# Performance work log

Measured on AMD Instinct MI355X. Metric: run time of the kernel, lower is better.

## Reference

```python
import jax, jax.numpy as jnp
import numpy as np
import math

# ---- hyperparameters taken verbatim from the source losses ----
NSAMPLE_REP = 20      # ballquery nsample in get_repulsion_loss
RADIUS_REP = 0.07     # ballquery radius in get_repulsion_loss
H_REP = 0.03          # kernel bandwidth h
PERCENTAGES = (0.004, 0.008, 0.01, 0.012, 0.016)
UNI_RADIUS = 1.0


def _gather(p, idx):
    # p: [B, N, 3], idx: [B, ...] int -> [B, ..., 3]  (pointops.grouping/gathering)
    return jax.vmap(lambda pts, i: pts[i])(p, idx)


def _ballquery(radius, nsample, q, p):
    # pointops.ballquery: for each query, first `nsample` point indices within
    # radius, padded with the first found index. q:[B,M,3], p:[B,N,3] -> [B,M,nsample]
    d = jnp.sum((q[:, :, None, :] - p[:, None, :, :]) ** 2, -1)  # [B,M,N]
    N = p.shape[1]
    keys = jnp.where(d <= radius * radius,
                     jnp.arange(N, dtype=jnp.int32)[None, None, :], N)
    idx = jnp.sort(keys, axis=-1)[..., :nsample]
    return jnp.where(idx >= N, idx[..., :1], idx)  # pad misses with first hit


def _fps(pcd, npoint):
    # pointops.furthestsampling on [B,N,3] -> [B,npoint] int32
    B, N, _ = pcd.shape
    bidx = jnp.arange(B)

    def step(carry, _):
        dist, far = carry                         # [B,N], [B]
        pt = pcd[bidx, far]                       # [B,3]
        d = jnp.sum((pcd - pt[:, None, :]) ** 2, -1)
        dist = jnp.minimum(dist, d)
        nxt = jnp.argmax(dist, -1).astype(jnp.int32)
        return (dist, nxt), far

    init = (jnp.full((B, N), 1e10, pcd.dtype), jnp.zeros((B,), jnp.int32))
    _, idxs = jax.lax.scan(step, init, None, length=npoint)
    return idxs.T  # [B, npoint]


def _repulsion_loss(pred):
    # pred: [B, N, 3]
    idx = _ballquery(RADIUS_REP, NSAMPLE_REP, pred, pred)   # [B,N,20], detached ints
    g = _gather(pred, idx) - pred[:, :, None, :]            # [B,N,20,3]
    dists = jnp.sum(g * g, -1)                              # [B,N,20]
    vals, _ = jax.lax.top_k(-dists, 5)                      # 5 smallest sq-dists
    d5 = jnp.maximum(-vals[:, :, 1:], 0.0)                  # drop self, ReLU
    ds = jnp.sqrt(d5)
    w = jnp.exp(-d5 / (H_REP * H_REP))
    return jnp.mean(RADIUS_REP - ds * w)


def _uniform_loss(pcd):
    # pcd: [B, N, 3]
    N = pcd.shape[1]
    npoint = int(N * 0.05)
    # FPS is called with identical args for every percentage -> compute once.
    fps_idx = _fps(jax.lax.stop_gradient(pcd), npoint)
    new_xyz = _gather(pcd, fps_idx)                          # [B,npoint,3]
    loss = jnp.zeros((), pcd.dtype)
    for p in PERCENTAGES:
        nsample = int(N * p)
        r = math.sqrt(p * UNI_RADIUS)
        disk_area = math.pi * UNI_RADIUS ** 2 * p / nsample
        expect_len = math.sqrt(2 * disk_area / 1.732)
        idx = _ballquery(r, nsample, new_xyz, pcd)           # [B,npoint,nsample]
        grouped = _gather(pcd, idx).reshape(-1, nsample, 3)  # [B*npoint,nsample,3]
        # knn_point(2, grouped, grouped): pairwise sq-dists inside each disk
        d = jnp.sum((grouped[:, :, None, :] - grouped[:, None, :, :]) ** 2, -1)
        vals, _ = jax.lax.top_k(-d, 2)
        ud = -vals[:, :, 1:]                                  # nearest non-self sqdist
        ud = jnp.sqrt(jnp.abs(ud + 1e-8))
        ud = jnp.mean(ud, -1)
        ud = (ud - expect_len) ** 2 / (expect_len + 1e-8)
        loss = loss + jnp.mean(ud) * (p * 100.0) ** 2
    return loss / len(PERCENTAGES)


def setup_inputs() -> dict:
    key = jax.random.key(0)
    # refined upsampled cloud: B=4, r*N = 4*2048 = 8192 points in [-1,1]^3
    pcd = jax.random.uniform(key, (4, 8192, 3), jnp.float32) * 2.0 - 1.0
    return {"pcd": pcd}


def reference(pcd):
    return jnp.stack([_uniform_loss(pcd), _repulsion_loss(pcd)])
```

## Files before the change

### kernel.cpp

```cpp
#include <hip/hip_runtime.h>
#include <hip/hip_bf16.h>
#include <cmath>
#include <cfloat>

#define BATCH 4
#define NPTS 8192
#define NPOINT 409
#define NBALLS (BATCH * NPOINT)
#define REP_NS 20
#define REP_SEG 8
#define SEG_LEN (NPTS / REP_SEG)
#define REP_TASKS 512
#define NTASKS (REP_TASKS + NBALLS)
#define NWORKERS 252

#define UW 96
#define UH (8 * UW)

#define WS_FPS_OFF 0
#define WS_REP_OFF 8192
#define WS_UNI_OFF 12288
#define WS_CNT_OFF 25600

typedef float v2f __attribute__((ext_vector_type(2)));

struct UniParams {
  float  thr[5];
  float  e[5];
  float  eden[5];
  int    ns[5];
};

template <int CTRL>
__device__ __forceinline__ unsigned long long dpp_max_u64(unsigned long long key) {
  const int lo = __builtin_amdgcn_update_dpp(
      0, (int)(unsigned)(key & 0xFFFFFFFFull), CTRL, 0xf, 0xf, true);
  const int hi = __builtin_amdgcn_update_dpp(
      0, (int)(unsigned)(key >> 32), CTRL, 0xf, 0xf, true);
  const unsigned long long ok =
      ((unsigned long long)(unsigned)hi << 32) | (unsigned)lo;
  return ok > key ? ok : key;
}

__device__ __forceinline__ void ins5(float v, float& t0, float& t1, float& t2,
                                     float& t3, float& t4) {
  if (v < t4) {
    t4 = v;
    if (t4 < t3) { float tmp = t3; t3 = t4; t4 = tmp; }
    if (t3 < t2) { float tmp = t2; t2 = t3; t3 = tmp; }
    if (t2 < t1) { float tmp = t1; t1 = t2; t2 = tmp; }
    if (t1 < t0) { float tmp = t0; t0 = t1; t1 = tmp; }
  }
}

__device__ __forceinline__ float rep_term(float d) {
  d = fmaxf(d, 0.0f);
  return 0.07f - sqrtf(d) * expf(-(d / 0.0009f));
}

__global__ __launch_bounds__(512, 2) void fused_kernel(const float* __restrict__ pcd,
                                                       int* __restrict__ fps_idx,
                                                       double* __restrict__ rep_part,
                                                       double* __restrict__ uni_part,
                                                       int* __restrict__ counter,
                                                       UniParams up, float rep_thr) {
  const int tid = threadIdx.x;
  const int lane = tid & 63;
  const int w = tid >> 6;
  extern __shared__ float smem[];

  __shared__ unsigned long long s_key[2][8];
  __shared__ float s_t5[REP_SEG][64][5];
  __shared__ float s_d0[REP_SEG][64];
  __shared__ int   s_cnt[REP_SEG][64];
  __shared__ float wx[8][UW], wy[8][UW], wz[8][UW], wd[8][UW];
  __shared__ int   s_wcnt[8];
  __shared__ float FX[UH], FY[UH], FZ[UH], FD[UH];
  __shared__ float CX[5][131], CY[5][131], CZ[5][131];
  __shared__ double dpart[8];
  __shared__ int s_task, s_qidx;

  if (blockIdx.x < BATCH) {
    const int b = blockIdx.x;
    const float* P = pcd + b * NPTS * 3;
    float* X = smem;
    float* Y = smem + NPTS;
    float* Z = smem + 2 * NPTS;

    for (int i = tid; i < NPTS; i += 512) {
      X[i] = P[i * 3 + 0];
      Y[i] = P[i * 3 + 1];
      Z[i] = P[i * 3 + 2];
    }

    v2f px[8], py[8], pz[8], dist[8];
    const int base = tid * 16;
#pragma unroll
    for (int k = 0; k < 8; k++) {
      const int i0 = (base + 2 * k) * 3;
      const int i1 = (base + 2 * k + 1) * 3;
      px[k] = (v2f){P[i0 + 0], P[i1 + 0]};
      py[k] = (v2f){P[i0 + 1], P[i1 + 1]};
      pz[k] = (v2f){P[i0 + 2], P[i1 + 2]};
      dist[k] = (v2f){1e10f, 1e10f};
    }
#pragma unroll
    for (int k = 0; k < 8; k++) {
      asm volatile("" : "+v"(px[k]), "+v"(py[k]), "+v"(pz[k]));
    }

    __syncthreads();

    int far = 0;
    float fx = X[0], fy = Y[0], fz = Z[0];
    for (int s = 0; s < NPOINT; s++) {
      if (tid == 0) {
        __hip_atomic_store(&fps_idx[b * NPOINT + s], far,
                           __ATOMIC_RELAXED, __HIP_MEMORY_SCOPE_AGENT);
      }

      const v2f fxv = (v2f){fx, fx};
      const v2f fyv = (v2f){fy, fy};
      const v2f fzv = (v2f){fz, fz};
      float best = -1.0f;
      int kb = 0;
#pragma unroll
      for (int k = 0; k < 8; k++) {
#pragma clang fp contract(off)
        const v2f dx = px[k] - fxv;
        const v2f dy = py[k] - fyv;
        const v2f dz = pz[k] - fzv;
        const v2f d  = (dx * dx + dy * dy) + dz * dz;
        const float n0 = fminf(dist[k].x, d.x);
        const float n1 = fminf(dist[k].y, d.y);
        dist[k].x = n0;
        dist[k].y = n1;
        if (n0 > best) { best = n0; kb = 2 * k; }
        if (n1 > best) { best = n1; kb = 2 * k + 1; }
      }
      const int bidx = base + kb;
      unsigned long long key =
          ((unsigned long long)__float_as_uint(best) << 32) |
          (unsigned long long)(0xFFFFFFFFu - (unsigned)bidx);

      key = dpp_max_u64<0x111>(key);
      key = dpp_max_u64<0x112>(key);
      key = dpp_max_u64<0x114>(key);
      key = dpp_max_u64<0x118>(key);
      key = dpp_max_u64<0x142>(key);
      key = dpp_max_u64<0x143>(key);

      const int par = s & 1;
      if (lane == 63) s_key[par][w] = key;
      __syncthreads();
      unsigned long long kbk = s_key[par][0];
#pragma unroll
      for (int w2 = 1; w2 < 8; w2++) {
        const unsigned long long kk = s_key[par][w2];
        if (kk > kbk) kbk = kk;
      }
      far = (int)(0xFFFFFFFFu - (unsigned)(kbk & 0xFFFFFFFFull));
      fx = X[far];
      fy = Y[far];
      fz = Z[far];
    }
    return;
  }

  const double wj_tab[5] = {0.16 / (5.0 * 1636.0 * 32.0),
                            0.64 / (5.0 * 1636.0 * 65.0),
                            1.0  / (5.0 * 1636.0 * 81.0),
                            1.44 / (5.0 * 1636.0 * 98.0),
                            2.56 / (5.0 * 1636.0 * 131.0)};

  while (true) {
    __syncthreads();
    if (tid == 0) s_task = atomicAdd(counter, 1);
    __syncthreads();
    const int t = s_task;
    if (t >= NTASKS) return;

    if (t < REP_TASKS) {
      const int b = t >> 7;
      const int q = ((t & 127) << 6) + lane;
      const float* P = pcd + b * NPTS * 3;

      const float qx = P[q * 3 + 0], qy = P[q * 3 + 1], qz = P[q * 3 + 2];

      int cnt = 0;
      float d0 = 0.0f;
      float t0 = FLT_MAX, t1 = FLT_MAX, t2 = FLT_MAX, t3 = FLT_MAX, t4 = FLT_MAX;

      const int wu = __builtin_amdgcn_readfirstlane(w);
      const float* S = P + wu * SEG_LEN * 3;
#pragma unroll 4
      for (int i = 0; i < SEG_LEN; i++) {
        const float x = S[i * 3 + 0];
        const float y = S[i * 3 + 1];
        const float z = S[i * 3 + 2];
        const float dx = qx - x, dy = qy - y, dz = qz - z;
        const float d = dx * dx + dy * dy + dz * dz;
        if (d <= rep_thr && cnt < REP_NS) {
          if (cnt == 0) d0 = d;
          ins5(d, t0, t1, t2, t3, t4);
          cnt++;
        }
      }

      s_t5[w][lane][0] = t0; s_t5[w][lane][1] = t1; s_t5[w][lane][2] = t2;
      s_t5[w][lane][3] = t3; s_t5[w][lane][4] = t4;
      s_d0[w][lane] = d0;
      s_cnt[w][lane] = cnt;
      __syncthreads();

      if (w == 0) {
        int total = 0;
        float fd0 = 0.0f;
        int first_seen = 0;
        float m0 = FLT_MAX, m1 = FLT_MAX, m2 = FLT_MAX, m3 = FLT_MAX, m4 = FLT_MAX;
#pragma unroll
        for (int sg = 0; sg < REP_SEG; sg++) {
          const int c = s_cnt[sg][lane];
          if (c > 0 && !first_seen) { fd0 = s_d0[sg][lane]; first_seen = 1; }
          total += c;
#pragma unroll
          for (int j = 0; j < 5; j++) ins5(s_t5[sg][lane][j], m0, m1, m2, m3, m4);
        }

        if (total > REP_NS) {
          int c2 = 0;
          m0 = FLT_MAX; m1 = FLT_MAX; m2 = FLT_MAX; m3 = FLT_MAX; m4 = FLT_MAX;
          for (int i = 0; i < NPTS && c2 < REP_NS; i++) {
            const float dx = qx - P[i * 3 + 0];
            const float dy = qy - P[i * 3 + 1];
            const float dz = qz - P[i * 3 + 2];
            const float d = dx * dx + dy * dy + dz * dz;
            if (d <= rep_thr) { ins5(d, m0, m1, m2, m3, m4); c2++; }
          }
        } else {
          for (int c = total; c < REP_NS; c++) ins5(fd0, m0, m1, m2, m3, m4);
        }

        float sum = rep_term(m1) + rep_term(m2) + rep_term(m3) + rep_term(m4);
#pragma unroll
        for (int off = 32; off >= 1; off >>= 1) sum += __shfl_down(sum, off);
        if (lane == 0) rep_part[t] = (double)sum;
      }
    } else {
      const int ball = t - REP_TASKS;
      const int b = ball / NPOINT;
      const float* P = pcd + b * NPTS * 3;

      if (tid == 0) {
        int v = __hip_atomic_load(&fps_idx[ball], __ATOMIC_RELAXED,
                                  __HIP_MEMORY_SCOPE_AGENT);
        while (v < 0) {
          __builtin_amdgcn_s_sleep(32);
          v = __hip_atomic_load(&fps_idx[ball], __ATOMIC_RELAXED,
                                __HIP_MEMORY_SCOPE_AGENT);
        }
        s_qidx = v;
      }
      __syncthreads();
      const int qidx = s_qidx;
      const float qx = P[qidx * 3 + 0], qy = P[qidx * 3 + 1], qz = P[qidx * 3 + 2];

      int wcnt = 0;
      const float* S = P + w * 1024 * 3;
      for (int it = 0; it < 16; it++) {
        const int j = it * 64 + lane;
        const float x = S[j * 3 + 0];
        const float y = S[j * 3 + 1];
        const float z = S[j * 3 + 2];
        const float dx = qx - x, dy = qy - y, dz = qz - z;
        const float d = dx * dx + dy * dy + dz * dz;
        const bool hit = (d <= up.thr[4]);
        const unsigned long long m = __ballot(hit);
        if (hit) {
          const int pos = wcnt + __popcll(m & ((1ull << lane) - 1ull));
          if (pos < UW) {
            wx[w][pos] = x; wy[w][pos] = y; wz[w][pos] = z; wd[w][pos] = d;
          }
        }
        wcnt += __popcll(m);
      }
      if (lane == 0) s_wcnt[w] = min(wcnt, UW);
      __syncthreads();

      int off = 0;
#pragma unroll
      for (int w2 = 0; w2 < 8; w2++) {
        if (w2 == w) break;
        off += s_wcnt[w2];
      }
      for (int i = lane; i < s_wcnt[w]; i += 64) {
        FX[off + i] = wx[w][i]; FY[off + i] = wy[w][i];
        FZ[off + i] = wz[w][i]; FD[off + i] = wd[w][i];
      }
      __syncthreads();
      int c = 0;
#pragma unroll
      for (int w2 = 0; w2 < 8; w2++) c += s_wcnt[w2];

      double local = 0.0;
      if (w < 5) {
        const int jp = w;
        const float thr = up.thr[jp];
        const int nsj = up.ns[jp];

        int cnt2 = 0;
        for (int bse = 0; bse < c; bse += 64) {
          const int e = bse + lane;
          const bool pred = (e < c) && (FD[e] <= thr);
          const unsigned long long m = __ballot(pred);
          if (pred) {
            const int pos = cnt2 + __popcll(m & ((1ull << lane) - 1ull));
            if (pos < nsj) {
              CX[jp][pos] = FX[e]; CY[jp][pos] = FY[e]; CZ[jp][pos] = FZ[e];
            }
          }
          cnt2 += __popcll(m);
        }
        const int cj = min(cnt2, nsj);
        const int pads = nsj - cj;
        const int istart = (pads > 0) ? 1 : 0;

        if (pads > 0 && lane == 0) {
          const float ud = sqrtf(fabsf(1e-8f));
          const float dd = ud - up.e[jp];
          const float tt = (dd * dd) / up.eden[jp];
          local += (double)tt * wj_tab[jp] * (double)(pads + 1);
        }

        for (int r = istart + lane; r < cj; r += 64) {
          const float xi = CX[jp][r], yi = CY[jp][r], zi = CZ[jp][r];
          float m2 = FLT_MAX;
          for (int e2 = 0; e2 < cj; e2++) {
            if (e2 == r) continue;
            const float dx = xi - CX[jp][e2];
            const float dy = yi - CY[jp][e2];
            const float dz = zi - CZ[jp][e2];
            const float d = dx * dx + dy * dy + dz * dz;
            if (d < m2) m2 = d;
          }
          const float ud = sqrtf(fabsf(m2 + 1e-8f));
          const float dd = ud - up.e[jp];
          const float tt = (dd * dd) / up.eden[jp];
          local += (double)tt * wj_tab[jp];
        }
      }

#pragma unroll
      for (int o = 32; o >= 1; o >>= 1) local += __shfl_down(local, o);
      if (lane == 0) dpart[w] = local;
      __syncthreads();
      if (tid == 0) {
        double u = 0.0;
#pragma unroll
        for (int w2 = 0; w2 < 8; w2++) u += dpart[w2];
        uni_part[ball] = u;
      }
    }
  }
}

__global__ __launch_bounds__(256) void fin_kernel(const double* __restrict__ rep_part,
                                                  const double* __restrict__ uni_part,
                                                  float* __restrict__ out) {
  __shared__ double sd[256];
  const int t = threadIdx.x;
  double u = 0.0, r = 0.0;
  for (int i = t; i < NBALLS; i += 256) u += uni_part[i];
  for (int i = t; i < REP_TASKS; i += 256) r += rep_part[i];

  sd[t] = u; __syncthreads();
  for (int s = 128; s > 0; s >>= 1) { if (t < s) sd[t] += sd[t + s]; __syncthreads(); }
  const double usum = sd[0];
  __syncthreads();
  sd[t] = r; __syncthreads();
  for (int s = 128; s > 0; s >>= 1) { if (t < s) sd[t] += sd[t + s]; __syncthreads(); }

  if (t == 0) {
    out[0] = (float)usum;
    out[1] = (float)(sd[0] * (1.0 / 131072.0));
  }
}

extern "C" void kernel_launch(void* const* d_in, const int* in_sizes, int n_in,
                              void* d_out, int out_size, void* d_ws, size_t ws_size,
                              hipStream_t stream) {
  (void)in_sizes; (void)n_in; (void)out_size; (void)ws_size;
  const float* pcd = (const float*)d_in[0];
  float* out = (float*)d_out;
  int*    fps      = (int*)((char*)d_ws + WS_FPS_OFF);
  double* rep_part = (double*)((char*)d_ws + WS_REP_OFF);
  double* uni_part = (double*)((char*)d_ws + WS_UNI_OFF);
  int*    counter  = (int*)((char*)d_ws + WS_CNT_OFF);

  const float rep_thr = (float)(0.07 * 0.07);

  UniParams up;
  const double ps[5] = {0.004, 0.008, 0.01, 0.012, 0.016};
  for (int j = 0; j < 5; j++) {
    const int ns = (int)(8192.0 * ps[j]);
    const double r = sqrt(ps[j]);
    up.thr[j] = (float)(r * r);
    const double disk = M_PI * ps[j] / (double)ns;
    const double el = sqrt(2.0 * disk / 1.732);
    up.e[j] = (float)el;
    up.eden[j] = (float)(el + 1e-8);
    up.ns[j] = ns;
  }

  hipMemsetAsync(fps, 0xFF, NBALLS * sizeof(int), stream);
  hipMemsetAsync(counter, 0, sizeof(int), stream);

  static const int kDynLds = NPTS * 3 * (int)sizeof(float);
  (void)hipFuncSetAttribute((const void*)fused_kernel,
                            hipFuncAttributeMaxDynamicSharedMemorySize, kDynLds);

  fused_kernel<<<BATCH + NWORKERS, 512, kDynLds, stream>>>(pcd, fps, rep_part,
                                                           uni_part, counter,
                                                           up, rep_thr);
  fin_kernel<<<1, 256, 0, stream>>>(rep_part, uni_part, out);
}
```

Baseline: 435.9 us.

## Simplify FPS argmax reduction and fold final reduction into last block

The FPS loop now reduces only the 32-bit max distance across the wavefront with DPP, then finds the winning lane via ballot and recovers its local index with a scan. This replaces the per-element best/index tracking and the 64-bit DPP key reduction. Separately, the final-sum kernel is removed: the last block to finish, detected with an atomic counter, performs the global reduction and writes the output. This saves one kernel launch at the cost of an extra atomic and fences.

```diff
diff --git a/kernel.cpp b/kernel.cpp
--- a/kernel.cpp
+++ b/kernel.cpp
@@ -13,6 +13,7 @@
 #define REP_TASKS 512
 #define NTASKS (REP_TASKS + NBALLS)
 #define NWORKERS 252
+#define NBLOCKS (BATCH + NWORKERS)
 
 #define UW 96
 #define UH (8 * UW)
@@ -32,14 +33,10 @@
 };
 
 template <int CTRL>
-__device__ __forceinline__ unsigned long long dpp_max_u64(unsigned long long key) {
-  const int lo = __builtin_amdgcn_update_dpp(
-      0, (int)(unsigned)(key & 0xFFFFFFFFull), CTRL, 0xf, 0xf, true);
-  const int hi = __builtin_amdgcn_update_dpp(
-      0, (int)(unsigned)(key >> 32), CTRL, 0xf, 0xf, true);
-  const unsigned long long ok =
-      ((unsigned long long)(unsigned)hi << 32) | (unsigned)lo;
-  return ok > key ? ok : key;
+__device__ __forceinline__ unsigned dpp_max_u32(unsigned v) {
+  const unsigned o = (unsigned)__builtin_amdgcn_update_dpp(
+      0, (int)v, CTRL, 0xf, 0xf, true);
+  return o > v ? o : v;
 }
 
 __device__ __forceinline__ void ins5(float v, float& t0, float& t1, float& t2,
@@ -63,6 +60,7 @@
                                                        double* __restrict__ rep_part,
                                                        double* __restrict__ uni_part,
                                                        int* __restrict__ counter,
+                                                       float* __restrict__ out,
                                                        UniParams up, float rep_thr) {
   const int tid = threadIdx.x;
   const int lane = tid & 63;
@@ -77,8 +75,8 @@
   __shared__ int   s_wcnt[8];
   __shared__ float FX[UH], FY[UH], FZ[UH], FD[UH];
   __shared__ float CX[5][131], CY[5][131], CZ[5][131];
-  __shared__ double dpart[8];
-  __shared__ int s_task, s_qidx;
+  __shared__ double dpart[8], rpart[8];
+  __shared__ int s_task, s_qidx, s_last;
 
   if (blockIdx.x < BATCH) {
     const int b = blockIdx.x;
@@ -122,8 +120,6 @@
       const v2f fxv = (v2f){fx, fx};
       const v2f fyv = (v2f){fy, fy};
       const v2f fzv = (v2f){fz, fz};
-      float best = -1.0f;
-      int kb = 0;
 #pragma unroll
       for (int k = 0; k < 8; k++) {
 #pragma clang fp contract(off)
@@ -131,28 +127,46 @@
         const v2f dy = py[k] - fyv;
         const v2f dz = pz[k] - fzv;
         const v2f d  = (dx * dx + dy * dy) + dz * dz;
-        const float n0 = fminf(dist[k].x, d.x);
-        const float n1 = fminf(dist[k].y, d.y);
-        dist[k].x = n0;
-        dist[k].y = n1;
-        if (n0 > best) { best = n0; kb = 2 * k; }
-        if (n1 > best) { best = n1; kb = 2 * k + 1; }
+        dist[k].x = fminf(dist[k].x, d.x);
+        dist[k].y = fminf(dist[k].y, d.y);
       }
-      const int bidx = base + kb;
-      unsigned long long key =
-          ((unsigned long long)__float_as_uint(best) << 32) |
-          (unsigned long long)(0xFFFFFFFFu - (unsigned)bidx);
-
-      key = dpp_max_u64<0x111>(key);
-      key = dpp_max_u64<0x112>(key);
-      key = dpp_max_u64<0x114>(key);
-      key = dpp_max_u64<0x118>(key);
-      key = dpp_max_u64<0x142>(key);
-      key = dpp_max_u64<0x143>(key);
-
+
+      const float m0 = fmaxf(fmaxf(dist[0].x, dist[0].y),
+                             fmaxf(dist[1].x, dist[1].y));
+      const float m1 = fmaxf(fmaxf(dist[2].x, dist[2].y),
+                             fmaxf(dist[3].x, dist[3].y));
+      const float m2 = fmaxf(fmaxf(dist[4].x, dist[4].y),
+                             fmaxf(dist[5].x, dist[5].y));
+      const float m3 = fmaxf(fmaxf(dist[6].x, dist[6].y),
+                             fmaxf(dist[7].x, dist[7].y));
+      const float tmax = fmaxf(fmaxf(m0, m1), fmaxf(m2, m3));
+
+      const unsigned tb = __float_as_uint(tmax);
+      unsigned rb = tb;
+      rb = dpp_max_u32<0x111>(rb);
+      rb = dpp_max_u32<0x112>(rb);
+      rb = dpp_max_u32<0x114>(rb);
+      rb = dpp_max_u32<0x118>(rb);
+      rb = dpp_max_u32<0x142>(rb);
+      rb = dpp_max_u32<0x143>(rb);
+      const unsigned wb = (unsigned)__builtin_amdgcn_readlane((int)rb, 63);
+
+      const unsigned long long hit = __ballot(tb == wb);
       const int par = s & 1;
-      if (lane == 63) s_key[par][w] = key;
+      if (tb == wb && (hit & ((1ull << lane) - 1ull)) == 0ull) {
+        const float wv = __uint_as_float(wb);
+        int li = 0;
+#pragma unroll
+        for (int j = 15; j >= 0; j--) {
+          const float v = (j & 1) ? dist[j >> 1].y : dist[j >> 1].x;
+          li = (v == wv) ? j : li;
+        }
+        const unsigned bidx = (unsigned)(base + li);
+        s_key[par][w] = ((unsigned long long)wb << 32) |
+                        (unsigned long long)(0xFFFFFFFFu - bidx);
+      }
       __syncthreads();
+
       unsigned long long kbk = s_key[par][0];
 #pragma unroll
       for (int w2 = 1; w2 < 8; w2++) {
@@ -164,225 +178,231 @@
       fy = Y[far];
       fz = Z[far];
     }
-    return;
+  } else {
+    const double wj_tab[5] = {0.16 / (5.0 * 1636.0 * 32.0),
+                              0.64 / (5.0 * 1636.0 * 65.0),
+                              1.0  / (5.0 * 1636.0 * 81.0),
+                              1.44 / (5.0 * 1636.0 * 98.0),
+                              2.56 / (5.0 * 1636.0 * 131.0)};
+
+    while (true) {
+      __syncthreads();
+      if (tid == 0) s_task = atomicAdd(counter, 1);
+      __syncthreads();
+      const int t = s_task;
+      if (t >= NTASKS) break;
+
+      if (t < REP_TASKS) {
+        const int b = t >> 7;
+        const int q = ((t & 127) << 6) + lane;
+        const float* P = pcd + b * NPTS * 3;
+
+        const float qx = P[q * 3 + 0], qy = P[q * 3 + 1], qz = P[q * 3 + 2];
+
+        int cnt = 0;
+        float d0 = 0.0f;
+        float t0 = FLT_MAX, t1 = FLT_MAX, t2 = FLT_MAX, t3 = FLT_MAX, t4 = FLT_MAX;
+
+        const int wu = __builtin_amdgcn_readfirstlane(w);
+        const float* S = P + wu * SEG_LEN * 3;
+#pragma unroll 4
+        for (int i = 0; i < SEG_LEN; i++) {
+          const float x = S[i * 3 + 0];
+          const float y = S[i * 3 + 1];
+          const float z = S[i * 3 + 2];
+          const float dx = qx - x, dy = qy - y, dz = qz - z;
+          const float d = dx * dx + dy * dy + dz * dz;
+          if (d <= rep_thr && cnt < REP_NS) {
+            if (cnt == 0) d0 = d;
+            ins5(d, t0, t1, t2, t3, t4);
+            cnt++;
+          }
+        }
+
+        s_t5[w][lane][0] = t0; s_t5[w][lane][1] = t1; s_t5[w][lane][2] = t2;
+        s_t5[w][lane][3] = t3; s_t5[w][lane][4] = t4;
+        s_d0[w][lane] = d0;
+        s_cnt[w][lane] = cnt;
+        __syncthreads();
+
+        if (w == 0) {
+          int total = 0;
+          float fd0 = 0.0f;
+          int first_seen = 0;
+          float n0 = FLT_MAX, n1 = FLT_MAX, n2 = FLT_MAX, n3 = FLT_MAX, n4 = FLT_MAX;
+#pragma unroll
+          for (int sg = 0; sg < REP_SEG; sg++) {
+            const int c = s_cnt[sg][lane];
+            if (c > 0 && !first_seen) { fd0 = s_d0[sg][lane]; first_seen = 1; }
+            total += c;
+#pragma unroll
+            for (int j = 0; j < 5; j++) ins5(s_t5[sg][lane][j], n0, n1, n2, n3, n4);
+          }
+
+          if (total > REP_NS) {
+            int c2 = 0;
+            n0 = FLT_MAX; n1 = FLT_MAX; n2 = FLT_MAX; n3 = FLT_MAX; n4 = FLT_MAX;
+            for (int i = 0; i < NPTS && c2 < REP_NS; i++) {
+              const float dx = qx - P[i * 3 + 0];
+              const float dy = qy - P[i * 3 + 1];
+              const float dz = qz - P[i * 3 + 2];
+              const float d = dx * dx + dy * dy + dz * dz;
+              if (d <= rep_thr) { ins5(d, n0, n1, n2, n3, n4); c2++; }
+            }
+          } else {
+            for (int c = total; c < REP_NS; c++) ins5(fd0, n0, n1, n2, n3, n4);
+          }
+
+          float sum = rep_term(n1) + rep_term(n2) + rep_term(n3) + rep_term(n4);
+#pragma unroll
+          for (int off = 32; off >= 1; off >>= 1) sum += __shfl_down(sum, off);
+          if (lane == 0) rep_part[t] = (double)sum;
+        }
+      } else {
+        const int ball = t - REP_TASKS;
+        const int b = ball / NPOINT;
+        const float* P = pcd + b * NPTS * 3;
+
+        if (tid == 0) {
+          int v = __hip_atomic_load(&fps_idx[ball], __ATOMIC_RELAXED,
+                                    __HIP_MEMORY_SCOPE_AGENT);
+          while (v < 0) {
+            __builtin_amdgcn_s_sleep(32);
+            v = __hip_atomic_load(&fps_idx[ball], __ATOMIC_RELAXED,
+                                  __HIP_MEMORY_SCOPE_AGENT);
+          }
+          s_qidx = v;
+        }
+        __syncthreads();
+        const int qidx = s_qidx;
+        const float qx = P[qidx * 3 + 0], qy = P[qidx * 3 + 1], qz = P[qidx * 3 + 2];
+
+        int wcnt = 0;
+        const float* S = P + w * 1024 * 3;
+        for (int it = 0; it < 16; it++) {
+          const int j = it * 64 + lane;
+          const float x = S[j * 3 + 0];
+          const float y = S[j * 3 + 1];
+          const float z = S[j * 3 + 2];
+          const float dx = qx - x, dy = qy - y, dz = qz - z;
+          const float d = dx * dx + dy * dy + dz * dz;
+          const bool hitp = (d <= up.thr[4]);
+          const unsigned long long m = __ballot(hitp);
+          if (hitp) {
+            const int pos = wcnt + __popcll(m & ((1ull << lane) - 1ull));
+            if (pos < UW) {
+              wx[w][pos] = x; wy[w][pos] = y; wz[w][pos] = z; wd[w][pos] = d;
+            }
+          }
+          wcnt += __popcll(m);
+        }
+        if (lane == 0) s_wcnt[w] = min(wcnt, UW);
+        __syncthreads();
+
+        int off = 0;
+#pragma unroll
+        for (int w2 = 0; w2 < 8; w2++) {
+          if (w2 == w) break;
+          off += s_wcnt[w2];
+        }
+        for (int i = lane; i < s_wcnt[w]; i += 64) {
+          FX[off + i] = wx[w][i]; FY[off + i] = wy[w][i];
+          FZ[off + i] = wz[w][i]; FD[off + i] = wd[w][i];
+        }
+        __syncthreads();
+        int c = 0;
+#pragma unroll
+        for (int w2 = 0; w2 < 8; w2++) c += s_wcnt[w2];
+
+        double local = 0.0;
+        if (w < 5) {
+          const int jp = w;
+          const float thr = up.thr[jp];
+          const int nsj = up.ns[jp];
+
+          int cnt2 = 0;
+          for (int bse = 0; bse < c; bse += 64) {
+            const int e = bse + lane;
+            const bool pred = (e < c) && (FD[e] <= thr);
+            const unsigned long long m = __ballot(pred);
+            if (pred) {
+              const int pos = cnt2 + __popcll(m & ((1ull << lane) - 1ull));
+              if (pos < nsj) {
+                CX[jp][pos] = FX[e]; CY[jp][pos] = FY[e]; CZ[jp][pos] = FZ[e];
+              }
+            }
+            cnt2 += __popcll(m);
+          }
+          const int cj = min(cnt2, nsj);
+          const int pads = nsj - cj;
+          const int istart = (pads > 0) ? 1 : 0;
+
+          if (pads > 0 && lane == 0) {
+            const float ud = sqrtf(fabsf(1e-8f));
+            const float dd = ud - up.e[jp];
+            const float tt = (dd * dd) / up.eden[jp];
+            local += (double)tt * wj_tab[jp] * (double)(pads + 1);
+          }
+
+          for (int r = istart + lane; r < cj; r += 64) {
+            const float xi = CX[jp][r], yi = CY[jp][r], zi = CZ[jp][r];
+            float mm = FLT_MAX;
+            for (int e2 = 0; e2 < cj; e2++) {
+              if (e2 == r) continue;
+              const float dx = xi - CX[jp][e2];
+              const float dy = yi - CY[jp][e2];
+              const float dz = zi - CZ[jp][e2];
+              const float d = dx * dx + dy * dy + dz * dz;
+              if (d < mm) mm = d;
+            }
+            const float ud = sqrtf(fabsf(mm + 1e-8f));
+            const float dd = ud - up.e[jp];
+            const float tt = (dd * dd) / up.eden[jp];
+            local += (double)tt * wj_tab[jp];
+          }
+        }
+
+#pragma unroll
+        for (int o = 32; o >= 1; o >>= 1) local += __shfl_down(local, o);
+        if (lane == 0) dpart[w] = local;
+        __syncthreads();
+        if (tid == 0) {
+          double u = 0.0;
+#pragma unroll
+          for (int w2 = 0; w2 < 8; w2++) u += dpart[w2];
+          uni_part[ball] = u;
+        }
+      }
+    }
   }
 
-  const double wj_tab[5] = {0.16 / (5.0 * 1636.0 * 32.0),
-                            0.64 / (5.0 * 1636.0 * 65.0),
-                            1.0  / (5.0 * 1636.0 * 81.0),
-                            1.44 / (5.0 * 1636.0 * 98.0),
-                            2.56 / (5.0 * 1636.0 * 131.0)};
-
-  while (true) {
+  __syncthreads();
+  if (tid == 0) {
+    __threadfence();
+    const int old = __hip_atomic_fetch_add(counter + 1, 1, __ATOMIC_ACQ_REL,
+                                           __HIP_MEMORY_SCOPE_AGENT);
+    s_last = (old == NBLOCKS - 1) ? 1 : 0;
+    if (s_last) __threadfence();
+  }
+  __syncthreads();
+  if (s_last) {
+    double u = 0.0, r = 0.0;
+    for (int i = tid; i < NBALLS; i += 512) u += uni_part[i];
+    for (int i = tid; i < REP_TASKS; i += 512) r += rep_part[i];
+#pragma unroll
+    for (int o = 32; o >= 1; o >>= 1) {
+      u += __shfl_down(u, o);
+      r += __shfl_down(r, o);
+    }
+    if (lane == 0) { dpart[w] = u; rpart[w] = r; }
     __syncthreads();
-    if (tid == 0) s_task = atomicAdd(counter, 1);
-    __syncthreads();
-    const int t = s_task;
-    if (t >= NTASKS) return;
-
-    if (t < REP_TASKS) {
-      const int b = t >> 7;
-      const int q = ((t & 127) << 6) + lane;
-      const float* P = pcd + b * NPTS * 3;
-
-      const float qx = P[q * 3 + 0], qy = P[q * 3 + 1], qz = P[q * 3 + 2];
-
-      int cnt = 0;
-      float d0 = 0.0f;
-      float t0 = FLT_MAX, t1 = FLT_MAX, t2 = FLT_MAX, t3 = FLT_MAX, t4 = FLT_MAX;
-
-      const int wu = __builtin_amdgcn_readfirstlane(w);
-      const float* S = P + wu * SEG_LEN * 3;
-#pragma unroll 4
-      for (int i = 0; i < SEG_LEN; i++) {
-        const float x = S[i * 3 + 0];
-        const float y = S[i * 3 + 1];
-        const float z = S[i * 3 + 2];
-        const float dx = qx - x, dy = qy - y, dz = qz - z;
-        const float d = dx * dx + dy * dy + dz * dz;
-        if (d <= rep_thr && cnt < REP_NS) {
-          if (cnt == 0) d0 = d;
-          ins5(d, t0, t1, t2, t3, t4);
-          cnt++;
-        }
-      }
-
-      s_t5[w][lane][0] = t0; s_t5[w][lane][1] = t1; s_t5[w][lane][2] = t2;
-      s_t5[w][lane][3] = t3; s_t5[w][lane][4] = t4;
-      s_d0[w][lane] = d0;
-      s_cnt[w][lane] = cnt;
-      __syncthreads();
-
-      if (w == 0) {
-        int total = 0;
-        float fd0 = 0.0f;
-        int first_seen = 0;
-        float m0 = FLT_MAX, m1 = FLT_MAX, m2 = FLT_MAX, m3 = FLT_MAX, m4 = FLT_MAX;
-#pragma unroll
-        for (int sg = 0; sg < REP_SEG; sg++) {
-          const int c = s_cnt[sg][lane];
-          if (c > 0 && !first_seen) { fd0 = s_d0[sg][lane]; first_seen = 1; }
-          total += c;
-#pragma unroll
-          for (int j = 0; j < 5; j++) ins5(s_t5[sg][lane][j], m0, m1, m2, m3, m4);
-        }
-
-        if (total > REP_NS) {
-          int c2 = 0;
-          m0 = FLT_MAX; m1 = FLT_MAX; m2 = FLT_MAX; m3 = FLT_MAX; m4 = FLT_MAX;
-          for (int i = 0; i < NPTS && c2 < REP_NS; i++) {
-            const float dx = qx - P[i * 3 + 0];
-            const float dy = qy - P[i * 3 + 1];
-            const float dz = qz - P[i * 3 + 2];
-            const float d = dx * dx + dy * dy + dz * dz;
-            if (d <= rep_thr) { ins5(d, m0, m1, m2, m3, m4); c2++; }
-          }
-        } else {
-          for (int c = total; c < REP_NS; c++) ins5(fd0, m0, m1, m2, m3, m4);
-        }
-
-        float sum = rep_term(m1) + rep_term(m2) + rep_term(m3) + rep_term(m4);
-#pragma unroll
-        for (int off = 32; off >= 1; off >>= 1) sum += __shfl_down(sum, off);
-        if (lane == 0) rep_part[t] = (double)sum;
-      }
-    } else {
-      const int ball = t - REP_TASKS;
-      const int b = ball / NPOINT;
-      const float* P = pcd + b * NPTS * 3;
-
-      if (tid == 0) {
-        int v = __hip_atomic_load(&fps_idx[ball], __ATOMIC_RELAXED,
-                                  __HIP_MEMORY_SCOPE_AGENT);
-        while (v < 0) {
-          __builtin_amdgcn_s_sleep(32);
-          v = __hip_atomic_load(&fps_idx[ball], __ATOMIC_RELAXED,
-                                __HIP_MEMORY_SCOPE_AGENT);
-        }
-        s_qidx = v;
-      }
-      __syncthreads();
-      const int qidx = s_qidx;
-      const float qx = P[qidx * 3 + 0], qy = P[qidx * 3 + 1], qz = P[qidx * 3 + 2];
-
-      int wcnt = 0;
-      const float* S = P + w * 1024 * 3;
-      for (int it = 0; it < 16; it++) {
-        const int j = it * 64 + lane;
-        const float x = S[j * 3 + 0];
-        const float y = S[j * 3 + 1];
-        const float z = S[j * 3 + 2];
-        const float dx = qx - x, dy = qy - y, dz = qz - z;
-        const float d = dx * dx + dy * dy + dz * dz;
-        const bool hit = (d <= up.thr[4]);
-        const unsigned long long m = __ballot(hit);
-        if (hit) {
-          const int pos = wcnt + __popcll(m & ((1ull << lane) - 1ull));
-          if (pos < UW) {
-            wx[w][pos] = x; wy[w][pos] = y; wz[w][pos] = z; wd[w][pos] = d;
-          }
-        }
-        wcnt += __popcll(m);
-      }
-      if (lane == 0) s_wcnt[w] = min(wcnt, UW);
-      __syncthreads();
-
-      int off = 0;
-#pragma unroll
-      for (int w2 = 0; w2 < 8; w2++) {
-        if (w2 == w) break;
-        off += s_wcnt[w2];
-      }
-      for (int i = lane; i < s_wcnt[w]; i += 64) {
-        FX[off + i] = wx[w][i]; FY[off + i] = wy[w][i];
-        FZ[off + i] = wz[w][i]; FD[off + i] = wd[w][i];
-      }
-      __syncthreads();
-      int c = 0;
-#pragma unroll
-      for (int w2 = 0; w2 < 8; w2++) c += s_wcnt[w2];
-
-      double local = 0.0;
-      if (w < 5) {
-        const int jp = w;
-        const float thr = up.thr[jp];
-        const int nsj = up.ns[jp];
-
-        int cnt2 = 0;
-        for (int bse = 0; bse < c; bse += 64) {
-          const int e = bse + lane;
-          const bool pred = (e < c) && (FD[e] <= thr);
-          const unsigned long long m = __ballot(pred);
-          if (pred) {
-            const int pos = cnt2 + __popcll(m & ((1ull << lane) - 1ull));
-            if (pos < nsj) {
-              CX[jp][pos] = FX[e]; CY[jp][pos] = FY[e]; CZ[jp][pos] = FZ[e];
-            }
-          }
-          cnt2 += __popcll(m);
-        }
-        const int cj = min(cnt2, nsj);
-        const int pads = nsj - cj;
-        const int istart = (pads > 0) ? 1 : 0;
-
-        if (pads > 0 && lane == 0) {
-          const float ud = sqrtf(fabsf(1e-8f));
-          const float dd = ud - up.e[jp];
-          const float tt = (dd * dd) / up.eden[jp];
-          local += (double)tt * wj_tab[jp] * (double)(pads + 1);
-        }
-
-        for (int r = istart + lane; r < cj; r += 64) {
-          const float xi = CX[jp][r], yi = CY[jp][r], zi = CZ[jp][r];
-          float m2 = FLT_MAX;
-          for (int e2 = 0; e2 < cj; e2++) {
-            if (e2 == r) continue;
-            const float dx = xi - CX[jp][e2];
-            const float dy = yi - CY[jp][e2];
-            const float dz = zi - CZ[jp][e2];
-            const float d = dx * dx + dy * dy + dz * dz;
-            if (d < m2) m2 = d;
-          }
-          const float ud = sqrtf(fabsf(m2 + 1e-8f));
-          const float dd = ud - up.e[jp];
-          const float tt = (dd * dd) / up.eden[jp];
-          local += (double)tt * wj_tab[jp];
-        }
-      }
-
-#pragma unroll
-      for (int o = 32; o >= 1; o >>= 1) local += __shfl_down(local, o);
-      if (lane == 0) dpart[w] = local;
-      __syncthreads();
-      if (tid == 0) {
-        double u = 0.0;
-#pragma unroll
-        for (int w2 = 0; w2 < 8; w2++) u += dpart[w2];
-        uni_part[ball] = u;
-      }
-    }
-  }
-}
-
-__global__ __launch_bounds__(256) void fin_kernel(const double* __restrict__ rep_part,
-                                                  const double* __restrict__ uni_part,
-                                                  float* __restrict__ out) {
-  __shared__ double sd[256];
-  const int t = threadIdx.x;
-  double u = 0.0, r = 0.0;
-  for (int i = t; i < NBALLS; i += 256) u += uni_part[i];
-  for (int i = t; i < REP_TASKS; i += 256) r += rep_part[i];
-
-  sd[t] = u; __syncthreads();
-  for (int s = 128; s > 0; s >>= 1) { if (t < s) sd[t] += sd[t + s]; __syncthreads(); }
-  const double usum = sd[0];
-  __syncthreads();
-  sd[t] = r; __syncthreads();
-  for (int s = 128; s > 0; s >>= 1) { if (t < s) sd[t] += sd[t + s]; __syncthreads(); }
-
-  if (t == 0) {
-    out[0] = (float)usum;
-    out[1] = (float)(sd[0] * (1.0 / 131072.0));
+    if (tid == 0) {
+      double us = 0.0, rs = 0.0;
+#pragma unroll
+      for (int w2 = 0; w2 < 8; w2++) { us += dpart[w2]; rs += rpart[w2]; }
+      out[0] = (float)us;
+      out[1] = (float)(rs * (1.0 / 131072.0));
+    }
   }
 }
 
@@ -413,14 +433,12 @@
   }
 
   hipMemsetAsync(fps, 0xFF, NBALLS * sizeof(int), stream);
-  hipMemsetAsync(counter, 0, sizeof(int), stream);
+  hipMemsetAsync(counter, 0, 2 * sizeof(int), stream);
 
   static const int kDynLds = NPTS * 3 * (int)sizeof(float);
   (void)hipFuncSetAttribute((const void*)fused_kernel,
                             hipFuncAttributeMaxDynamicSharedMemorySize, kDynLds);
 
-  fused_kernel<<<BATCH + NWORKERS, 512, kDynLds, stream>>>(pcd, fps, rep_part,
-                                                           uni_part, counter,
-                                                           up, rep_thr);
-  fin_kernel<<<1, 256, 0, stream>>>(rep_part, uni_part, out);
+  fused_kernel<<<NBLOCKS, 512, kDynLds, stream>>>(pcd, fps, rep_part, uni_part,
+                                                  counter, out, up, rep_thr);
 }
```

New measurement: 413.9 us. 5.1% less time.
